# Kernel optimization log

Hardware: AMD Instinct MI355X
Metric: run time of the kernel (lower is better)

The kernel has to match this reference:

```python
import jax, jax.numpy as jnp
import numpy as np

EMB = 8
HID = 64
B = 1000
T = 512
N = (B * T) // 5  # events per source; sources partition the (batch,time) grid

_KEYS = ["ccba", "cdtx", "cust", "dp", "remit"]
_NUMS = {"ccba": 8, "cdtx": 1, "cust": 1, "dp": 2, "remit": 1}
_CATS = {"ccba": 0, "cdtx": 2, "cust": 3, "dp": 8, "remit": 1}
_VOCAB = {"ccba": 0, "cdtx": 179, "cust": 37, "dp": 435, "remit": 5}


def setup_inputs() -> dict:
    ks = iter(jax.random.split(jax.random.key(0), 64))
    rng = np.random.default_rng(0)
    chunks = np.split(rng.permutation(B * T), 5)
    d = {}
    for k5, ch in zip(_KEYS, chunks):
        d[k5 + "_num"] = jax.random.normal(next(ks), (N, _NUMS[k5]), jnp.float32)
        if _CATS[k5] > 0:
            d[k5 + "_cat"] = jax.random.randint(next(ks), (N, _CATS[k5]), 0, _VOCAB[k5])
            d[k5 + "_tab"] = jax.random.normal(next(ks), (_VOCAB[k5], EMB), jnp.float32) * 0.1
        d[k5 + "_bi"] = jnp.asarray(ch // T, jnp.int32)
        d[k5 + "_ti"] = jnp.asarray(ch % T, jnp.int32)
        in_dim = _CATS[k5] * EMB + _NUMS[k5]
        d[k5 + "_W"] = jax.random.normal(next(ks), (in_dim, HID), jnp.float32) * np.float32(1.0 / np.sqrt(in_dim))
        d[k5 + "_b"] = jnp.zeros((HID,), jnp.float32)
    # LSTM: 2 layers x 2 directions, hidden 64, proj_size 1 -> layer1 input is 2
    for l, insz in [(0, HID), (1, 2)]:
        d[f"Wih{l}"] = jax.random.normal(next(ks), (2, 4 * HID, insz), jnp.float32) * 0.05
        d[f"Whh{l}"] = jax.random.normal(next(ks), (2, 4 * HID, 1), jnp.float32) * 0.05
        d[f"Whr{l}"] = jax.random.normal(next(ks), (2, 1, HID), jnp.float32) * 0.05
        d[f"bih{l}"] = jnp.zeros((2, 4 * HID), jnp.float32)
        d[f"bhh{l}"] = jnp.zeros((2, 4 * HID), jnp.float32)
    d["length"] = T
    d["batch_size"] = B
    return d


def _embed(num, cat, tab, W, b):
    # FeatureEmbedder: concat(categorical embeddings, numeric) -> Linear(hidden)
    x = num if cat is None else jnp.concatenate([tab[cat].reshape(cat.shape[0], -1), num], axis=-1)
    return x @ W + b


def _lstm_dir(x, Wih, Whh, Whr, bih, bhh, reverse):
    Bx = x.shape[0]
    H = Whr.shape[1]
    p = Whr.shape[0]
    bias = bih + bhh

    def step(carry, xt):
        h, c = carry  # h: [B,p] projected hidden, c: [B,H] cell
        g = xt @ Wih.T + h @ Whh.T + bias
        i, f, gg, o = jnp.split(g, 4, axis=-1)  # PyTorch gate order i,f,g,o
        c = jax.nn.sigmoid(f) * c + jax.nn.sigmoid(i) * jnp.tanh(gg)
        h = (jax.nn.sigmoid(o) * jnp.tanh(c)) @ Whr.T  # proj_size projection
        return (h, c), h

    init = (jnp.zeros((Bx, p), x.dtype), jnp.zeros((Bx, H), x.dtype))
    _, ys = jax.lax.scan(step, init, jnp.swapaxes(x, 0, 1), reverse=reverse)
    return jnp.swapaxes(ys, 0, 1)  # [B,T,p]


def _bilstm(x, Wih, Whh, Whr, bih, bhh):
    fwd = _lstm_dir(x, Wih[0], Whh[0], Whr[0], bih[0], bhh[0], False)
    bwd = _lstm_dir(x, Wih[1], Whh[1], Whr[1], bih[1], bhh[1], True)
    return jnp.concatenate([fwd, bwd], axis=-1)


def _forward(a):
    feat = jnp.zeros((a["batch_size"], a["length"], HID), jnp.float32)
    for k5 in _KEYS:
        v = _embed(a[k5 + "_num"], a.get(k5 + "_cat"), a.get(k5 + "_tab"), a[k5 + "_W"], a[k5 + "_b"])
        feat = feat.at[a[k5 + "_bi"], a[k5 + "_ti"]].set(v)  # scatter-assemble padded tensor
    h = _bilstm(feat, a["Wih0"], a["Whh0"], a["Whr0"], a["bih0"], a["bhh0"])
    h = _bilstm(h, a["Wih1"], a["Whh1"], a["Whr1"], a["bih1"], a["bhh1"])
    return h.mean(axis=2)  # [B,T]


def reference(ccba_num, ccba_bi, ccba_ti, ccba_W, ccba_b,
              cdtx_num, cdtx_cat, cdtx_tab, cdtx_bi, cdtx_ti, cdtx_W, cdtx_b,
              cust_num, cust_cat, cust_tab, cust_bi, cust_ti, cust_W, cust_b,
              dp_num, dp_cat, dp_tab, dp_bi, dp_ti, dp_W, dp_b,
              remit_num, remit_cat, remit_tab, remit_bi, remit_ti, remit_W, remit_b,
              Wih0, Whh0, Whr0, bih0, bhh0, Wih1, Whh1, Whr1, bih1, bhh1,
              length, batch_size):
    return _forward(dict(locals()))
```

## Files before the change

kernel.cpp:

```cpp
#include <hip/hip_runtime.h>
#include <cstdint>
#include <cstddef>

#define TLEN 512
#define BATCH 1000
#define NEV 102400
#define HID 64

__device__ __forceinline__ float fast_rcp(float x) {
#if __has_builtin(__builtin_amdgcn_rcpf)
    return __builtin_amdgcn_rcpf(x);
#else
    return 1.0f / x;
#endif
}
__device__ __forceinline__ float sigm(float x) { return fast_rcp(1.0f + __expf(-x)); }
__device__ __forceinline__ float tanh_f(float x) { return fmaf(2.0f, sigm(2.0f * x), -1.0f); }


__global__ __launch_bounds__(512) void compose_kernel(
    const float* __restrict__ W0, const float* __restrict__ B0,
    const float* __restrict__ W1, const float* __restrict__ B1,
    const float* __restrict__ W2, const float* __restrict__ B2,
    const float* __restrict__ W3, const float* __restrict__ B3,
    const float* __restrict__ W4, const float* __restrict__ B4,
    const float* __restrict__ Wih, const float* __restrict__ bih,
    const float* __restrict__ bhh, float* __restrict__ wp)
{
    const int col = threadIdx.x;
    const int row = blockIdx.x;
    const float* srcW; const float* srcB; int base, IND;
    if (row < 9)        { srcW = W0; srcB = B0; base = 0;   IND = 8;  }
    else if (row < 27)  { srcW = W1; srcB = B1; base = 9;   IND = 17; }
    else if (row < 53)  { srcW = W2; srcB = B2; base = 27;  IND = 25; }
    else if (row < 120) { srcW = W3; srcB = B3; base = 53;  IND = 66; }
    else                { srcW = W4; srcB = B4; base = 120; IND = 9;  }
    const int j = row - base;
    const float* xrow = (j < IND) ? (srcW + (size_t)j * 64) : srcB;
    const float* wr = Wih + (size_t)col * 64;
    float acc = 0.0f;
#pragma unroll
    for (int h2 = 0; h2 < 64; ++h2) acc = fmaf(xrow[h2], wr[h2], acc);
    if (j == IND) acc += bih[col] + bhh[col];
    wp[(size_t)row * 512 + col] = acc;
}

template<int NNUM, int NCAT>
__global__ __launch_bounds__(512) void project_kernel(
    const float* __restrict__ num, const int* __restrict__ cat,
    const float* __restrict__ tab, const int* __restrict__ bi,
    const int* __restrict__ ti, const float* __restrict__ wp,
    float* __restrict__ gpre)
{
    constexpr int IND = NCAT * 8 + NNUM;
    const int col = threadIdx.x;
    float wcol[IND];
#pragma unroll
    for (int j = 0; j < IND; ++j) wcol[j] = wp[(size_t)j * 512 + col];
    const float bcol = wp[(size_t)IND * 512 + col];

    for (int ev = blockIdx.x; ev < NEV; ev += gridDim.x) {
        const int pos = bi[ev] * TLEN + ti[ev];
        float acc = bcol;
#pragma unroll
        for (int c0 = 0; c0 < NCAT; ++c0) {
            const int idx = cat[ev * NCAT + c0];
            const float* tr = tab + (size_t)idx * 8;
#pragma unroll
            for (int u = 0; u < 8; ++u)
                acc = fmaf(tr[u], wcol[c0 * 8 + u], acc);
        }
#pragma unroll
        for (int u = 0; u < NNUM; ++u)
            acc = fmaf(num[(size_t)ev * NNUM + u], wcol[NCAT * 8 + u], acc);
        gpre[(size_t)pos * 512 + col] = acc;
    }
}

__global__ __launch_bounds__(256) void rec0_kernel(
    const float* __restrict__ gpre, const float* __restrict__ Whh,
    const float* __restrict__ Whr, float* __restrict__ h0)
{
    const int wv = threadIdx.x >> 6, lane = threadIdx.x & 63;
    const int p = blockIdx.x * 4 + wv;
    const int b = p >> 1, dir = p & 1;

    float whh4[4];
#pragma unroll
    for (int k = 0; k < 4; ++k) whh4[k] = Whh[dir * 256 + k * 64 + lane];
    const float whr = Whr[dir * HID + lane];

    const float* gb = gpre + (size_t)dir * 256 + lane;
    float* h0p = h0 + (size_t)b * TLEN * 2 + dir;

    auto addr = [&](int t) -> const float* {
        int tc = t < TLEN ? t : TLEN - 1;
        int tt = dir ? (TLEN - 1 - tc) : tc;
        return gb + ((size_t)(b * TLEN + tt)) * 512;
    };

    float A[4], B[4];
    {
        const float* pa = addr(0); const float* pb = addr(1);
#pragma unroll
        for (int k = 0; k < 4; ++k) { A[k] = pa[k * 64]; B[k] = pb[k * 64]; }
    }
    float h = 0.0f, c = 0.0f;

    for (int t = 0; t < TLEN; t += 2) {
        float C[4], D[4];
        const float* pc = addr(t + 2); const float* pd = addr(t + 3);
#pragma unroll
        for (int k = 0; k < 4; ++k) { C[k] = pc[k * 64]; D[k] = pd[k * 64]; }

        {
            float gi = fmaf(whh4[0], h, A[0]);
            float gf = fmaf(whh4[1], h, A[1]);
            float gg = fmaf(whh4[2], h, A[2]);
            float go = fmaf(whh4[3], h, A[3]);
            c = sigm(gf) * c + sigm(gi) * tanh_f(gg);
            float pp = sigm(go) * tanh_f(c) * whr;
#pragma unroll
            for (int off = 1; off < 64; off <<= 1) pp += __shfl_xor(pp, off, 64);
            h = pp;
            int tt = dir ? (TLEN - 1 - t) : t;
            if (lane == 0) h0p[(size_t)tt * 2] = h;
        }
        {
            float gi = fmaf(whh4[0], h, B[0]);
            float gf = fmaf(whh4[1], h, B[1]);
            float gg = fmaf(whh4[2], h, B[2]);
            float go = fmaf(whh4[3], h, B[3]);
            c = sigm(gf) * c + sigm(gi) * tanh_f(gg);
            float pp = sigm(go) * tanh_f(c) * whr;
#pragma unroll
            for (int off = 1; off < 64; off <<= 1) pp += __shfl_xor(pp, off, 64);
            h = pp;
            int tt = dir ? (TLEN - 2 - t) : (t + 1);
            if (lane == 0) h0p[(size_t)tt * 2] = h;
        }
#pragma unroll
        for (int k = 0; k < 4; ++k) { A[k] = C[k]; B[k] = D[k]; }
    }
}

__global__ __launch_bounds__(256) void lstm1_kernel(
    const float* __restrict__ h0, const float* __restrict__ Wih,
    const float* __restrict__ Whh, const float* __restrict__ Whr,
    const float* __restrict__ bih, const float* __restrict__ bhh,
    float* __restrict__ h1)
{
    int w = threadIdx.x >> 6, lane = threadIdx.x & 63;
    int p = blockIdx.x * 4 + w;
    int b = p >> 1, dir = p & 1;

    float wi0[4], wi1[4], whh[4], bias[4];
#pragma unroll
    for (int k = 0; k < 4; ++k) {
        int r = k * 64 + lane;
        wi0[k] = Wih[(size_t)(dir * 256 + r) * 2 + 0];
        wi1[k] = Wih[(size_t)(dir * 256 + r) * 2 + 1];
        whh[k] = Whh[dir * 256 + r];
        bias[k] = bih[dir * 256 + r] + bhh[dir * 256 + r];
    }
    float whr = Whr[dir * HID + lane];
    float h = 0.0f, c = 0.0f;
    const float* hb = h0 + (size_t)b * TLEN * 2;

    auto xat = [&](int t) -> float2 {
        int tc = t < TLEN ? t : TLEN - 1;
        int tt = dir ? (TLEN - 1 - tc) : tc;
        return *(const float2*)(hb + (size_t)tt * 2);
    };

    float2 xA = xat(0), xB = xat(1);
    for (int t = 0; t < TLEN; t += 2) {
        float2 xC = xat(t + 2), xD = xat(t + 3);
        {
            float g[4];
#pragma unroll
            for (int k = 0; k < 4; ++k)
                g[k] = fmaf(whh[k], h, fmaf(wi1[k], xA.y, fmaf(wi0[k], xA.x, bias[k])));
            c = sigm(g[1]) * c + sigm(g[0]) * tanh_f(g[2]);
            float pp = sigm(g[3]) * tanh_f(c) * whr;
#pragma unroll
            for (int off = 1; off < 64; off <<= 1) pp += __shfl_xor(pp, off, 64);
            h = pp;
            int tt = dir ? (TLEN - 1 - t) : t;
            if (lane == 0) h1[((size_t)b * TLEN + tt) * 2 + dir] = h;
        }
        {
            float g[4];
#pragma unroll
            for (int k = 0; k < 4; ++k)
                g[k] = fmaf(whh[k], h, fmaf(wi1[k], xB.y, fmaf(wi0[k], xB.x, bias[k])));
            c = sigm(g[1]) * c + sigm(g[0]) * tanh_f(g[2]);
            float pp = sigm(g[3]) * tanh_f(c) * whr;
#pragma unroll
            for (int off = 1; off < 64; off <<= 1) pp += __shfl_xor(pp, off, 64);
            h = pp;
            int tt = dir ? (TLEN - 2 - t) : (t + 1);
            if (lane == 0) h1[((size_t)b * TLEN + tt) * 2 + dir] = h;
        }
        xA = xC; xB = xD;
    }
}

__global__ __launch_bounds__(256) void mean_kernel(
    const float2* __restrict__ h1, float* __restrict__ out)
{
    int i = blockIdx.x * 256 + threadIdx.x;
    if (i < BATCH * TLEN) {
        float2 v = h1[i];
        out[i] = 0.5f * (v.x + v.y);
    }
}

__global__ __launch_bounds__(256) void embed_kernel(
    const float* __restrict__ num, const int* __restrict__ cat,
    const float* __restrict__ tab, const int* __restrict__ bi,
    const int* __restrict__ ti, const float* __restrict__ W,
    const float* __restrict__ bvec, float* __restrict__ feat,
    int n_num, int n_cat)
{
    int e = blockIdx.x * 4 + (threadIdx.x >> 6);
    int hh = threadIdx.x & 63;
    if (e >= NEV) return;
    float acc = bvec[hh];
    int j = 0;
    for (int c = 0; c < n_cat; ++c) {
        int idx = cat[e * n_cat + c];
        const float* trow = tab + (size_t)idx * 8;
#pragma unroll
        for (int u = 0; u < 8; ++u)
            acc = fmaf(trow[u], W[(j + u) * HID + hh], acc);
        j += 8;
    }
    for (int u = 0; u < n_num; ++u)
        acc = fmaf(num[(size_t)e * n_num + u], W[(j + u) * HID + hh], acc);
    int pos = bi[e] * TLEN + ti[e];
    feat[(size_t)pos * HID + hh] = acc;
}

__global__ __launch_bounds__(256, 2) void lstm0_kernel(
    const float* __restrict__ feat, const float* __restrict__ Wih,
    const float* __restrict__ Whh, const float* __restrict__ Whr,
    const float* __restrict__ bih, const float* __restrict__ bhh,
    float* __restrict__ h0)
{
    const int b0 = blockIdx.x * 4;
    const int dir = blockIdx.y;
    const int tid = threadIdx.x, lane = tid & 63, wv = tid >> 6;

    const float* wrow = Wih + (size_t)(dir * 256 + tid) * HID;
    float4 w[16];
#pragma unroll
    for (int i = 0; i < 16; ++i) w[i] = ((const float4*)wrow)[i];
    const float whh = Whh[dir * 256 + tid];
    const float bias = bih[dir * 256 + tid] + bhh[dir * 256 + tid];
    const float whr = Whr[dir * HID + lane];

    __shared__ float4 featb[2][4][16];
    __shared__ float gbuf[4][256];
    __shared__ __align__(16) float hbuf[4];

    float c = 0.0f;
    const float* fb = feat + (size_t)(b0 + wv) * TLEN * HID;
    float* h0b = h0 + ((size_t)(b0 + wv) * TLEN) * 2 + dir;

    const int t0 = dir ? (TLEN - 1) : 0;
    ((float*)featb[0][wv])[lane] = fb[(size_t)t0 * HID + lane];
    if (tid < 4) hbuf[tid] = 0.0f;
    __syncthreads();

    for (int t = 0; t < TLEN; ++t) {
        const int buf = t & 1;
        const int tt = dir ? (TLEN - 1 - t) : t;
        float nf = 0.0f;
        const int tn = dir ? (TLEN - 2 - t) : (t + 1);
        const bool pf = (t < TLEN - 1);
        if (pf) nf = fb[(size_t)tn * HID + lane];
        const float4 hp = *(const float4*)hbuf;
        float a0 = fmaf(whh, hp.x, bias);
        float a1 = fmaf(whh, hp.y, bias);
        float a2 = fmaf(whh, hp.z, bias);
        float a3 = fmaf(whh, hp.w, bias);
#pragma unroll
        for (int i = 0; i < 16; ++i) {
            float4 f0 = featb[buf][0][i];
            float4 f1 = featb[buf][1][i];
            float4 f2 = featb[buf][2][i];
            float4 f3 = featb[buf][3][i];
            a0 = fmaf(f0.x, w[i].x, a0); a0 = fmaf(f0.y, w[i].y, a0);
            a0 = fmaf(f0.z, w[i].z, a0); a0 = fmaf(f0.w, w[i].w, a0);
            a1 = fmaf(f1.x, w[i].x, a1); a1 = fmaf(f1.y, w[i].y, a1);
            a1 = fmaf(f1.z, w[i].z, a1); a1 = fmaf(f1.w, w[i].w, a1);
            a2 = fmaf(f2.x, w[i].x, a2); a2 = fmaf(f2.y, w[i].y, a2);
            a2 = fmaf(f2.z, w[i].z, a2); a2 = fmaf(f2.w, w[i].w, a2);
            a3 = fmaf(f3.x, w[i].x, a3); a3 = fmaf(f3.y, w[i].y, a3);
            a3 = fmaf(f3.z, w[i].z, a3); a3 = fmaf(f3.w, w[i].w, a3);
        }
        gbuf[0][tid] = a0;
        gbuf[1][tid] = a1;
        gbuf[2][tid] = a2;
        gbuf[3][tid] = a3;
        if (pf) ((float*)featb[1 - buf][wv])[lane] = nf;
        __syncthreads();
        const float gi = gbuf[wv][lane];
        const float gf = gbuf[wv][64 + lane];
        const float gg = gbuf[wv][128 + lane];
        const float go = gbuf[wv][192 + lane];
        c = sigm(gf) * c + sigm(gi) * tanh_f(gg);
        float p = sigm(go) * tanh_f(c) * whr;
#pragma unroll
        for (int off = 1; off < 64; off <<= 1) p += __shfl_xor(p, off, 64);
        if (lane == 0) {
            hbuf[wv] = p;
            h0b[(size_t)tt * 2] = p;
        }
        __syncthreads();
    }
}

extern "C" void kernel_launch(void* const* d_in, const int* in_sizes, int n_in,
                              void* d_out, int out_size, void* d_ws, size_t ws_size,
                              hipStream_t stream)
{
    const float* ccba_num = (const float*)d_in[0];
    const int*   ccba_bi  = (const int*)d_in[1];
    const int*   ccba_ti  = (const int*)d_in[2];
    const float* ccba_W   = (const float*)d_in[3];
    const float* ccba_b   = (const float*)d_in[4];
    const float* cdtx_num = (const float*)d_in[5];
    const int*   cdtx_cat = (const int*)d_in[6];
    const float* cdtx_tab = (const float*)d_in[7];
    const int*   cdtx_bi  = (const int*)d_in[8];
    const int*   cdtx_ti  = (const int*)d_in[9];
    const float* cdtx_W   = (const float*)d_in[10];
    const float* cdtx_b   = (const float*)d_in[11];
    const float* cust_num = (const float*)d_in[12];
    const int*   cust_cat = (const int*)d_in[13];
    const float* cust_tab = (const float*)d_in[14];
    const int*   cust_bi  = (const int*)d_in[15];
    const int*   cust_ti  = (const int*)d_in[16];
    const float* cust_W   = (const float*)d_in[17];
    const float* cust_b   = (const float*)d_in[18];
    const float* dp_num   = (const float*)d_in[19];
    const int*   dp_cat   = (const int*)d_in[20];
    const float* dp_tab   = (const float*)d_in[21];
    const int*   dp_bi    = (const int*)d_in[22];
    const int*   dp_ti    = (const int*)d_in[23];
    const float* dp_W     = (const float*)d_in[24];
    const float* dp_b     = (const float*)d_in[25];
    const float* remit_num = (const float*)d_in[26];
    const int*   remit_cat = (const int*)d_in[27];
    const float* remit_tab = (const float*)d_in[28];
    const int*   remit_bi  = (const int*)d_in[29];
    const int*   remit_ti  = (const int*)d_in[30];
    const float* remit_W   = (const float*)d_in[31];
    const float* remit_b   = (const float*)d_in[32];
    const float* Wih0 = (const float*)d_in[33];
    const float* Whh0 = (const float*)d_in[34];
    const float* Whr0 = (const float*)d_in[35];
    const float* bih0 = (const float*)d_in[36];
    const float* bhh0 = (const float*)d_in[37];
    const float* Wih1 = (const float*)d_in[38];
    const float* Whh1 = (const float*)d_in[39];
    const float* Whr1 = (const float*)d_in[40];
    const float* bih1 = (const float*)d_in[41];
    const float* bhh1 = (const float*)d_in[42];

    float* out = (float*)d_out;
    dim3 blk(256);

    const size_t GPRE_BYTES = (size_t)512000 * 512 * 4;
    const size_t H0_OFF = GPRE_BYTES;
    const size_t H1_OFF = H0_OFF + 4096000;
    const size_t WP_OFF = H1_OFF + 4096000;
    const size_t NEED   = WP_OFF + 130 * 512 * 4;

    if (ws_size >= NEED) {
        char* ws = (char*)d_ws;
        float* gpre = (float*)ws;
        float* h0   = (float*)(ws + H0_OFF);
        float* h1   = (float*)(ws + H1_OFF);
        float* wp   = (float*)(ws + WP_OFF);

        compose_kernel<<<130, 512, 0, stream>>>(
            ccba_W, ccba_b, cdtx_W, cdtx_b, cust_W, cust_b,
            dp_W, dp_b, remit_W, remit_b, Wih0, bih0, bhh0, wp);

        project_kernel<8, 0><<<512, 512, 0, stream>>>(ccba_num, nullptr, nullptr, ccba_bi, ccba_ti, wp + (size_t)0 * 512, gpre);
        project_kernel<1, 2><<<512, 512, 0, stream>>>(cdtx_num, cdtx_cat, cdtx_tab, cdtx_bi, cdtx_ti, wp + (size_t)9 * 512, gpre);
        project_kernel<1, 3><<<512, 512, 0, stream>>>(cust_num, cust_cat, cust_tab, cust_bi, cust_ti, wp + (size_t)27 * 512, gpre);
        project_kernel<2, 8><<<512, 512, 0, stream>>>(dp_num, dp_cat, dp_tab, dp_bi, dp_ti, wp + (size_t)53 * 512, gpre);
        project_kernel<1, 1><<<512, 512, 0, stream>>>(remit_num, remit_cat, remit_tab, remit_bi, remit_ti, wp + (size_t)120 * 512, gpre);

        rec0_kernel<<<500, blk, 0, stream>>>(gpre, Whh0, Whr0, h0);
        lstm1_kernel<<<500, blk, 0, stream>>>(h0, Wih1, Whh1, Whr1, bih1, bhh1, h1);
        mean_kernel<<<(BATCH * TLEN + 255) / 256, blk, 0, stream>>>((const float2*)h1, out);
    } else {
        char* ws = (char*)d_ws;
        float* feat = (float*)ws;
        float* h0   = (float*)(ws + 131072000);
        float* h1   = (float*)(ws + 135168000);
        int eg = (NEV + 3) / 4;
        embed_kernel<<<eg, blk, 0, stream>>>(ccba_num, nullptr, nullptr, ccba_bi, ccba_ti, ccba_W, ccba_b, feat, 8, 0);
        embed_kernel<<<eg, blk, 0, stream>>>(cdtx_num, cdtx_cat, cdtx_tab, cdtx_bi, cdtx_ti, cdtx_W, cdtx_b, feat, 1, 2);
        embed_kernel<<<eg, blk, 0, stream>>>(cust_num, cust_cat, cust_tab, cust_bi, cust_ti, cust_W, cust_b, feat, 1, 3);
        embed_kernel<<<eg, blk, 0, stream>>>(dp_num, dp_cat, dp_tab, dp_bi, dp_ti, dp_W, dp_b, feat, 2, 8);
        embed_kernel<<<eg, blk, 0, stream>>>(remit_num, remit_cat, remit_tab, remit_bi, remit_ti, remit_W, remit_b, feat, 1, 1);
        lstm0_kernel<<<dim3(BATCH / 4, 2), blk, 0, stream>>>(feat, Wih0, Whh0, Whr0, bih0, bhh0, h0);
        lstm1_kernel<<<500, blk, 0, stream>>>(h0, Wih1, Whh1, Whr1, bih1, bhh1, h1);
        mean_kernel<<<(BATCH * TLEN + 255) / 256, blk, 0, stream>>>((const float2*)h1, out);
    }
}
```

Measured before the change: 1.562 ms.

## Chunk gate precompute by batch ranges to fit workspace, merge projection launches

Replaces the two workspace-dependent paths with a single chunked pipeline. A bucketing kernel groups events by batch chunk, then for each chunk one fused launch projects all five sources into a per-chunk gate buffer, followed by the recurrence over that chunk. This removes the slow fallback path and lets the precomputed-gate approach run even when the workspace is small, with software prefetching of the next event's inputs. The cost is an atomic bucketing pass, a memset and extra serial launches per chunk, and the lists are capped so overflow would silently drop events.

```diff
diff --git a/kernel.cpp b/kernel.cpp
--- a/kernel.cpp
+++ b/kernel.cpp
@@ -17,6 +17,13 @@
 __device__ __forceinline__ float sigm(float x) { return fast_rcp(1.0f + __expf(-x)); }
 __device__ __forceinline__ float tanh_f(float x) { return fmaf(2.0f, sigm(2.0f * x), -1.0f); }
 
+struct Src {
+    const float* num;
+    const int*   cat;
+    const float* tab;
+    const int*   bi;
+    const int*   ti;
+};
 
 __global__ __launch_bounds__(512) void compose_kernel(
     const float* __restrict__ W0, const float* __restrict__ B0,
@@ -45,58 +52,123 @@
     wp[(size_t)row * 512 + col] = acc;
 }
 
+__global__ __launch_bounds__(256) void build_lists(
+    Src s0, Src s1, Src s2, Src s3, Src s4,
+    int NB, int chunks, int cap, int* __restrict__ cnt, int* __restrict__ evlist)
+{
+    int g = blockIdx.x * 256 + threadIdx.x;
+    if (g >= 5 * NEV) return;
+    int src = g / NEV, e = g - src * NEV;
+    const int* bi = (src == 0) ? s0.bi : (src == 1) ? s1.bi :
+                    (src == 2) ? s2.bi : (src == 3) ? s3.bi : s4.bi;
+    int c = bi[e] / NB;
+    int slot = atomicAdd(&cnt[src * chunks + c], 1);
+    if (slot < cap) evlist[(size_t)(src * chunks + c) * cap + slot] = e;
+}
+
 template<int NNUM, int NCAT>
-__global__ __launch_bounds__(512) void project_kernel(
-    const float* __restrict__ num, const int* __restrict__ cat,
-    const float* __restrict__ tab, const int* __restrict__ bi,
-    const int* __restrict__ ti, const float* __restrict__ wp,
-    float* __restrict__ gpre)
+__device__ __forceinline__ void project_body(
+    const Src s, const float* __restrict__ wp, float* __restrict__ gpre,
+    const int* __restrict__ list, const int n, const int b0)
 {
     constexpr int IND = NCAT * 8 + NNUM;
+    constexpr int NC = NCAT > 0 ? NCAT : 1;
     const int col = threadIdx.x;
     float wcol[IND];
 #pragma unroll
     for (int j = 0; j < IND; ++j) wcol[j] = wp[(size_t)j * 512 + col];
     const float bcol = wp[(size_t)IND * 512 + col];
 
-    for (int ev = blockIdx.x; ev < NEV; ev += gridDim.x) {
-        const int pos = bi[ev] * TLEN + ti[ev];
+    int i = (int)blockIdx.x;
+    if (i >= n) return;
+    const int stride = (int)gridDim.x;
+
+    int ev = list[i];
+    int nbi = s.bi[ev], nti = s.ti[ev];
+    int ncat[NC]; float nnum[NNUM];
+#pragma unroll
+    for (int c = 0; c < NCAT; ++c) ncat[c] = s.cat[ev * NCAT + c];
+#pragma unroll
+    for (int u = 0; u < NNUM; ++u) nnum[u] = s.num[(size_t)ev * NNUM + u];
+
+    while (true) {
+        const int cbi = nbi, cti = nti;
+        int ccat[NC]; float cnum[NNUM];
+#pragma unroll
+        for (int c = 0; c < NCAT; ++c) ccat[c] = ncat[c];
+#pragma unroll
+        for (int u = 0; u < NNUM; ++u) cnum[u] = nnum[u];
+
+        const int ni = i + stride;
+        if (ni < n) {
+            ev = list[ni];
+            nbi = s.bi[ev]; nti = s.ti[ev];
+#pragma unroll
+            for (int c = 0; c < NCAT; ++c) ncat[c] = s.cat[ev * NCAT + c];
+#pragma unroll
+            for (int u = 0; u < NNUM; ++u) nnum[u] = s.num[(size_t)ev * NNUM + u];
+        }
+
         float acc = bcol;
 #pragma unroll
-        for (int c0 = 0; c0 < NCAT; ++c0) {
-            const int idx = cat[ev * NCAT + c0];
-            const float* tr = tab + (size_t)idx * 8;
+        for (int c = 0; c < NCAT; ++c) {
+            const float* tr = s.tab + (size_t)ccat[c] * 8;
 #pragma unroll
             for (int u = 0; u < 8; ++u)
-                acc = fmaf(tr[u], wcol[c0 * 8 + u], acc);
+                acc = fmaf(tr[u], wcol[c * 8 + u], acc);
         }
 #pragma unroll
         for (int u = 0; u < NNUM; ++u)
-            acc = fmaf(num[(size_t)ev * NNUM + u], wcol[NCAT * 8 + u], acc);
-        gpre[(size_t)pos * 512 + col] = acc;
-    }
-}
-
-__global__ __launch_bounds__(256) void rec0_kernel(
+            acc = fmaf(cnum[u], wcol[NCAT * 8 + u], acc);
+
+        gpre[((size_t)(cbi - b0) * TLEN + cti) * 512 + col] = acc;
+
+        i = ni;
+        if (i >= n) break;
+    }
+}
+
+__global__ __launch_bounds__(512) void project_all(
+    Src s0, Src s1, Src s2, Src s3, Src s4,
+    const float* __restrict__ wp, float* __restrict__ gpre,
+    const int* __restrict__ cnt, const int* __restrict__ evlist,
+    int cap, int chunkIdx, int chunks, int b0)
+{
+    const int src = blockIdx.y;
+    int n = cnt[src * chunks + chunkIdx];
+    if (n > cap) n = cap;
+    const int* list = evlist + (size_t)(src * chunks + chunkIdx) * cap;
+    switch (src) {
+        case 0: project_body<8, 0>(s0, wp,              gpre, list, n, b0); break;
+        case 1: project_body<1, 2>(s1, wp + 9 * 512,    gpre, list, n, b0); break;
+        case 2: project_body<1, 3>(s2, wp + 27 * 512,   gpre, list, n, b0); break;
+        case 3: project_body<2, 8>(s3, wp + 53 * 512,   gpre, list, n, b0); break;
+        default: project_body<1, 1>(s4, wp + 120 * 512, gpre, list, n, b0); break;
+    }
+}
+
+__global__ __launch_bounds__(256) void rec0_chunk(
     const float* __restrict__ gpre, const float* __restrict__ Whh,
-    const float* __restrict__ Whr, float* __restrict__ h0)
+    const float* __restrict__ Whr, float* __restrict__ h0,
+    int b0, int nb)
 {
     const int wv = threadIdx.x >> 6, lane = threadIdx.x & 63;
     const int p = blockIdx.x * 4 + wv;
-    const int b = p >> 1, dir = p & 1;
+    if (p >= nb * 2) return;
+    const int bl = p >> 1, dir = p & 1;
 
     float whh4[4];
 #pragma unroll
     for (int k = 0; k < 4; ++k) whh4[k] = Whh[dir * 256 + k * 64 + lane];
     const float whr = Whr[dir * HID + lane];
 
-    const float* gb = gpre + (size_t)dir * 256 + lane;
-    float* h0p = h0 + (size_t)b * TLEN * 2 + dir;
+    const float* gb = gpre + (size_t)bl * TLEN * 512 + dir * 256 + lane;
+    float* h0p = h0 + (size_t)(b0 + bl) * TLEN * 2 + dir;
 
     auto addr = [&](int t) -> const float* {
         int tc = t < TLEN ? t : TLEN - 1;
         int tt = dir ? (TLEN - 1 - tc) : tc;
-        return gb + ((size_t)(b * TLEN + tt)) * 512;
+        return gb + (size_t)tt * 512;
     };
 
     float A[4], B[4];
@@ -216,149 +288,30 @@
     }
 }
 
-__global__ __launch_bounds__(256) void embed_kernel(
-    const float* __restrict__ num, const int* __restrict__ cat,
-    const float* __restrict__ tab, const int* __restrict__ bi,
-    const int* __restrict__ ti, const float* __restrict__ W,
-    const float* __restrict__ bvec, float* __restrict__ feat,
-    int n_num, int n_cat)
-{
-    int e = blockIdx.x * 4 + (threadIdx.x >> 6);
-    int hh = threadIdx.x & 63;
-    if (e >= NEV) return;
-    float acc = bvec[hh];
-    int j = 0;
-    for (int c = 0; c < n_cat; ++c) {
-        int idx = cat[e * n_cat + c];
-        const float* trow = tab + (size_t)idx * 8;
-#pragma unroll
-        for (int u = 0; u < 8; ++u)
-            acc = fmaf(trow[u], W[(j + u) * HID + hh], acc);
-        j += 8;
-    }
-    for (int u = 0; u < n_num; ++u)
-        acc = fmaf(num[(size_t)e * n_num + u], W[(j + u) * HID + hh], acc);
-    int pos = bi[e] * TLEN + ti[e];
-    feat[(size_t)pos * HID + hh] = acc;
-}
-
-__global__ __launch_bounds__(256, 2) void lstm0_kernel(
-    const float* __restrict__ feat, const float* __restrict__ Wih,
-    const float* __restrict__ Whh, const float* __restrict__ Whr,
-    const float* __restrict__ bih, const float* __restrict__ bhh,
-    float* __restrict__ h0)
-{
-    const int b0 = blockIdx.x * 4;
-    const int dir = blockIdx.y;
-    const int tid = threadIdx.x, lane = tid & 63, wv = tid >> 6;
-
-    const float* wrow = Wih + (size_t)(dir * 256 + tid) * HID;
-    float4 w[16];
-#pragma unroll
-    for (int i = 0; i < 16; ++i) w[i] = ((const float4*)wrow)[i];
-    const float whh = Whh[dir * 256 + tid];
-    const float bias = bih[dir * 256 + tid] + bhh[dir * 256 + tid];
-    const float whr = Whr[dir * HID + lane];
-
-    __shared__ float4 featb[2][4][16];
-    __shared__ float gbuf[4][256];
-    __shared__ __align__(16) float hbuf[4];
-
-    float c = 0.0f;
-    const float* fb = feat + (size_t)(b0 + wv) * TLEN * HID;
-    float* h0b = h0 + ((size_t)(b0 + wv) * TLEN) * 2 + dir;
-
-    const int t0 = dir ? (TLEN - 1) : 0;
-    ((float*)featb[0][wv])[lane] = fb[(size_t)t0 * HID + lane];
-    if (tid < 4) hbuf[tid] = 0.0f;
-    __syncthreads();
-
-    for (int t = 0; t < TLEN; ++t) {
-        const int buf = t & 1;
-        const int tt = dir ? (TLEN - 1 - t) : t;
-        float nf = 0.0f;
-        const int tn = dir ? (TLEN - 2 - t) : (t + 1);
-        const bool pf = (t < TLEN - 1);
-        if (pf) nf = fb[(size_t)tn * HID + lane];
-        const float4 hp = *(const float4*)hbuf;
-        float a0 = fmaf(whh, hp.x, bias);
-        float a1 = fmaf(whh, hp.y, bias);
-        float a2 = fmaf(whh, hp.z, bias);
-        float a3 = fmaf(whh, hp.w, bias);
-#pragma unroll
-        for (int i = 0; i < 16; ++i) {
-            float4 f0 = featb[buf][0][i];
-            float4 f1 = featb[buf][1][i];
-            float4 f2 = featb[buf][2][i];
-            float4 f3 = featb[buf][3][i];
-            a0 = fmaf(f0.x, w[i].x, a0); a0 = fmaf(f0.y, w[i].y, a0);
-            a0 = fmaf(f0.z, w[i].z, a0); a0 = fmaf(f0.w, w[i].w, a0);
-            a1 = fmaf(f1.x, w[i].x, a1); a1 = fmaf(f1.y, w[i].y, a1);
-            a1 = fmaf(f1.z, w[i].z, a1); a1 = fmaf(f1.w, w[i].w, a1);
-            a2 = fmaf(f2.x, w[i].x, a2); a2 = fmaf(f2.y, w[i].y, a2);
-            a2 = fmaf(f2.z, w[i].z, a2); a2 = fmaf(f2.w, w[i].w, a2);
-            a3 = fmaf(f3.x, w[i].x, a3); a3 = fmaf(f3.y, w[i].y, a3);
-            a3 = fmaf(f3.z, w[i].z, a3); a3 = fmaf(f3.w, w[i].w, a3);
-        }
-        gbuf[0][tid] = a0;
-        gbuf[1][tid] = a1;
-        gbuf[2][tid] = a2;
-        gbuf[3][tid] = a3;
-        if (pf) ((float*)featb[1 - buf][wv])[lane] = nf;
-        __syncthreads();
-        const float gi = gbuf[wv][lane];
-        const float gf = gbuf[wv][64 + lane];
-        const float gg = gbuf[wv][128 + lane];
-        const float go = gbuf[wv][192 + lane];
-        c = sigm(gf) * c + sigm(gi) * tanh_f(gg);
-        float p = sigm(go) * tanh_f(c) * whr;
-#pragma unroll
-        for (int off = 1; off < 64; off <<= 1) p += __shfl_xor(p, off, 64);
-        if (lane == 0) {
-            hbuf[wv] = p;
-            h0b[(size_t)tt * 2] = p;
-        }
-        __syncthreads();
-    }
-}
-
 extern "C" void kernel_launch(void* const* d_in, const int* in_sizes, int n_in,
                               void* d_out, int out_size, void* d_ws, size_t ws_size,
                               hipStream_t stream)
 {
-    const float* ccba_num = (const float*)d_in[0];
-    const int*   ccba_bi  = (const int*)d_in[1];
-    const int*   ccba_ti  = (const int*)d_in[2];
-    const float* ccba_W   = (const float*)d_in[3];
-    const float* ccba_b   = (const float*)d_in[4];
-    const float* cdtx_num = (const float*)d_in[5];
-    const int*   cdtx_cat = (const int*)d_in[6];
-    const float* cdtx_tab = (const float*)d_in[7];
-    const int*   cdtx_bi  = (const int*)d_in[8];
-    const int*   cdtx_ti  = (const int*)d_in[9];
-    const float* cdtx_W   = (const float*)d_in[10];
-    const float* cdtx_b   = (const float*)d_in[11];
-    const float* cust_num = (const float*)d_in[12];
-    const int*   cust_cat = (const int*)d_in[13];
-    const float* cust_tab = (const float*)d_in[14];
-    const int*   cust_bi  = (const int*)d_in[15];
-    const int*   cust_ti  = (const int*)d_in[16];
-    const float* cust_W   = (const float*)d_in[17];
-    const float* cust_b   = (const float*)d_in[18];
-    const float* dp_num   = (const float*)d_in[19];
-    const int*   dp_cat   = (const int*)d_in[20];
-    const float* dp_tab   = (const float*)d_in[21];
-    const int*   dp_bi    = (const int*)d_in[22];
-    const int*   dp_ti    = (const int*)d_in[23];
-    const float* dp_W     = (const float*)d_in[24];
-    const float* dp_b     = (const float*)d_in[25];
-    const float* remit_num = (const float*)d_in[26];
-    const int*   remit_cat = (const int*)d_in[27];
-    const float* remit_tab = (const float*)d_in[28];
-    const int*   remit_bi  = (const int*)d_in[29];
-    const int*   remit_ti  = (const int*)d_in[30];
-    const float* remit_W   = (const float*)d_in[31];
-    const float* remit_b   = (const float*)d_in[32];
+    Src s0 = { (const float*)d_in[0], nullptr, nullptr,
+               (const int*)d_in[1], (const int*)d_in[2] };
+    const float* ccba_W = (const float*)d_in[3];
+    const float* ccba_b = (const float*)d_in[4];
+    Src s1 = { (const float*)d_in[5], (const int*)d_in[6], (const float*)d_in[7],
+               (const int*)d_in[8], (const int*)d_in[9] };
+    const float* cdtx_W = (const float*)d_in[10];
+    const float* cdtx_b = (const float*)d_in[11];
+    Src s2 = { (const float*)d_in[12], (const int*)d_in[13], (const float*)d_in[14],
+               (const int*)d_in[15], (const int*)d_in[16] };
+    const float* cust_W = (const float*)d_in[17];
+    const float* cust_b = (const float*)d_in[18];
+    Src s3 = { (const float*)d_in[19], (const int*)d_in[20], (const float*)d_in[21],
+               (const int*)d_in[22], (const int*)d_in[23] };
+    const float* dp_W = (const float*)d_in[24];
+    const float* dp_b = (const float*)d_in[25];
+    Src s4 = { (const float*)d_in[26], (const int*)d_in[27], (const float*)d_in[28],
+               (const int*)d_in[29], (const int*)d_in[30] };
+    const float* remit_W = (const float*)d_in[31];
+    const float* remit_b = (const float*)d_in[32];
     const float* Wih0 = (const float*)d_in[33];
     const float* Whh0 = (const float*)d_in[34];
     const float* Whr0 = (const float*)d_in[35];
@@ -369,49 +322,54 @@
     const float* Whr1 = (const float*)d_in[40];
     const float* bih1 = (const float*)d_in[41];
     const float* bhh1 = (const float*)d_in[42];
-
     float* out = (float*)d_out;
-    dim3 blk(256);
-
-    const size_t GPRE_BYTES = (size_t)512000 * 512 * 4;
-    const size_t H0_OFF = GPRE_BYTES;
-    const size_t H1_OFF = H0_OFF + 4096000;
-    const size_t WP_OFF = H1_OFF + 4096000;
-    const size_t NEED   = WP_OFF + 130 * 512 * 4;
-
-    if (ws_size >= NEED) {
-        char* ws = (char*)d_ws;
-        float* gpre = (float*)ws;
-        float* h0   = (float*)(ws + H0_OFF);
-        float* h1   = (float*)(ws + H1_OFF);
-        float* wp   = (float*)(ws + WP_OFF);
-
-        compose_kernel<<<130, 512, 0, stream>>>(
-            ccba_W, ccba_b, cdtx_W, cdtx_b, cust_W, cust_b,
-            dp_W, dp_b, remit_W, remit_b, Wih0, bih0, bhh0, wp);
-
-        project_kernel<8, 0><<<512, 512, 0, stream>>>(ccba_num, nullptr, nullptr, ccba_bi, ccba_ti, wp + (size_t)0 * 512, gpre);
-        project_kernel<1, 2><<<512, 512, 0, stream>>>(cdtx_num, cdtx_cat, cdtx_tab, cdtx_bi, cdtx_ti, wp + (size_t)9 * 512, gpre);
-        project_kernel<1, 3><<<512, 512, 0, stream>>>(cust_num, cust_cat, cust_tab, cust_bi, cust_ti, wp + (size_t)27 * 512, gpre);
-        project_kernel<2, 8><<<512, 512, 0, stream>>>(dp_num, dp_cat, dp_tab, dp_bi, dp_ti, wp + (size_t)53 * 512, gpre);
-        project_kernel<1, 1><<<512, 512, 0, stream>>>(remit_num, remit_cat, remit_tab, remit_bi, remit_ti, wp + (size_t)120 * 512, gpre);
-
-        rec0_kernel<<<500, blk, 0, stream>>>(gpre, Whh0, Whr0, h0);
-        lstm1_kernel<<<500, blk, 0, stream>>>(h0, Wih1, Whh1, Whr1, bih1, bhh1, h1);
-        mean_kernel<<<(BATCH * TLEN + 255) / 256, blk, 0, stream>>>((const float2*)h1, out);
-    } else {
-        char* ws = (char*)d_ws;
-        float* feat = (float*)ws;
-        float* h0   = (float*)(ws + 131072000);
-        float* h1   = (float*)(ws + 135168000);
-        int eg = (NEV + 3) / 4;
-        embed_kernel<<<eg, blk, 0, stream>>>(ccba_num, nullptr, nullptr, ccba_bi, ccba_ti, ccba_W, ccba_b, feat, 8, 0);
-        embed_kernel<<<eg, blk, 0, stream>>>(cdtx_num, cdtx_cat, cdtx_tab, cdtx_bi, cdtx_ti, cdtx_W, cdtx_b, feat, 1, 2);
-        embed_kernel<<<eg, blk, 0, stream>>>(cust_num, cust_cat, cust_tab, cust_bi, cust_ti, cust_W, cust_b, feat, 1, 3);
-        embed_kernel<<<eg, blk, 0, stream>>>(dp_num, dp_cat, dp_tab, dp_bi, dp_ti, dp_W, dp_b, feat, 2, 8);
-        embed_kernel<<<eg, blk, 0, stream>>>(remit_num, remit_cat, remit_tab, remit_bi, remit_ti, remit_W, remit_b, feat, 1, 1);
-        lstm0_kernel<<<dim3(BATCH / 4, 2), blk, 0, stream>>>(feat, Wih0, Whh0, Whr0, bih0, bhh0, h0);
-        lstm1_kernel<<<500, blk, 0, stream>>>(h0, Wih1, Whh1, Whr1, bih1, bhh1, h1);
-        mean_kernel<<<(BATCH * TLEN + 255) / 256, blk, 0, stream>>>((const float2*)h1, out);
-    }
-}
+
+    const size_t MiB = 1048576;
+    int NB = 1000, chunks = 1, cap = NEV + 8192;
+    size_t lists_b = 0;
+    for (int it = 0; it < 6; ++it) {
+        chunks = (BATCH + NB - 1) / NB;
+        NB = (BATCH + chunks - 1) / chunks;
+        cap = NEV / chunks + 8192;
+        lists_b = ((size_t)5 * chunks * cap * 4 + 255) & ~(size_t)255;
+        size_t need = (size_t)NB * MiB + lists_b + 512 + 4096000 * 2 + 266240 + 1024;
+        if (need <= ws_size) break;
+        size_t fixed = lists_b + 512 + 4096000 * 2 + 266240 + 1024;
+        size_t avail = ws_size > fixed ? ws_size - fixed : MiB;
+        int nb_new = (int)(avail / MiB);
+        if (nb_new >= NB) nb_new = NB - 1;
+        if (nb_new < 2) nb_new = 2;
+        NB = nb_new;
+    }
+
+    char* p = (char*)d_ws;
+    float* gpre  = (float*)p;
+    size_t off   = (size_t)NB * MiB;
+    int*   evlist = (int*)(p + off);   off += lists_b;
+    int*   cnt    = (int*)(p + off);   off += ((size_t)5 * chunks * 4 + 255) & ~(size_t)255;
+    float* h0     = (float*)(p + off); off += 4096000;
+    float* h1     = (float*)(p + off); off += 4096000;
+    float* wp     = (float*)(p + off);
+
+    compose_kernel<<<130, 512, 0, stream>>>(
+        ccba_W, ccba_b, cdtx_W, cdtx_b, cust_W, cust_b,
+        dp_W, dp_b, remit_W, remit_b, Wih0, bih0, bhh0, wp);
+
+    hipMemsetAsync(cnt, 0, (size_t)5 * chunks * 4, stream);
+    build_lists<<<(5 * NEV + 255) / 256, 256, 0, stream>>>(
+        s0, s1, s2, s3, s4, NB, chunks, cap, cnt, evlist);
+
+    for (int ck = 0; ck < chunks; ++ck) {
+        const int b0 = ck * NB;
+        const int nb = (BATCH - b0) < NB ? (BATCH - b0) : NB;
+        project_all<<<dim3(256, 5), 512, 0, stream>>>(
+            s0, s1, s2, s3, s4, wp, gpre, cnt, evlist, cap, ck, chunks, b0);
+        rec0_chunk<<<(nb * 2 + 3) / 4, 256, 0, stream>>>(
+            gpre, Whh0, Whr0, h0, b0, nb);
+    }
+
+    lstm1_kernel<<<(BATCH * 2) / 4, 256, 0, stream>>>(
+        h0, Wih1, Whh1, Whr1, bih1, bhh1, h1);
+    mean_kernel<<<(BATCH * TLEN + 255) / 256, 256, 0, stream>>>(
+        (const float2*)h1, out);
+}
```

New measurement: 4.485 ms. 187% more time.
